# Kernel optimization log

Measured on AMD Instinct MI355X. Metric: run time of the kernel, lower is better.

The kernel has to match this reference:

```python
import jax, jax.numpy as jnp
import numpy as np

B, C, N, E, F = 8, 4, 2048, 512, 2048
EPS = 1e-5
MASK_SCALE = 5.0


def layer_norm(x, gamma, beta):
    mu = jnp.mean(x, axis=-1, keepdims=True)
    var = jnp.mean(jnp.square(x - mu), axis=-1, keepdims=True)
    return (x - mu) * jax.lax.rsqrt(var + EPS) * gamma + beta


def setup_inputs() -> dict:
    key = jax.random.key(0)
    ks = jax.random.split(key, 8)
    src = jax.random.normal(ks[0], (B, C, N, E), dtype=jnp.float32)
    key_padding_mask = jax.random.uniform(ks[1], (B, N), dtype=jnp.float32)
    # FFN params (torch Linear default init scale ~ U(-1/sqrt(fan_in), +))
    W1 = jax.random.normal(ks[2], (E, F), dtype=jnp.float32) / np.sqrt(E)
    b1 = jnp.zeros((F,), dtype=jnp.float32)
    W2 = jax.random.normal(ks[3], (F, E), dtype=jnp.float32) / np.sqrt(F)
    b2 = jnp.zeros((E,), dtype=jnp.float32)
    g1 = jnp.ones((E,), dtype=jnp.float32)
    be1 = jnp.zeros((E,), dtype=jnp.float32)
    g2 = jnp.ones((E,), dtype=jnp.float32)
    be2 = jnp.zeros((E,), dtype=jnp.float32)
    return {"src": src, "key_padding_mask": key_padding_mask,
            "W1": W1, "b1": b1, "W2": W2, "b2": b2,
            "g1": g1, "be1": be1, "g2": g2, "be2": be2}


def reference(src, key_padding_mask, W1, b1, W2, b2, g1, be1, g2, be2):
    # src: [B, C, N, E]; channels batched into one fused attention call
    scale = 1.0 / jnp.sqrt(jnp.asarray(src.shape[-1], src.dtype))
    scores = jnp.einsum('bcne,bcme->bcnm', src, src) * scale  # [B,C,N,N]
    scores = scores - key_padding_mask[:, None, None, :] * MASK_SCALE
    attn = jax.nn.softmax(scores, axis=-1)
    attn_out = jnp.einsum('bcnm,bcme->bcne', attn, src)
    # residual + norm1 (dropout is identity at eval)
    src2 = layer_norm(src + attn_out, g1, be1)
    # feedforward: Linear -> ReLU -> Linear
    ff = jax.nn.relu(jnp.einsum('bcne,ef->bcnf', src2, W1) + b1)
    ff = jnp.einsum('bcnf,fe->bcne', ff, W2) + b2
    out = layer_norm(src2 + ff, g2, be2)
    return out
```

## Files before the change

kernel.cpp:

```cpp
#include <hip/hip_runtime.h>
#include <stdint.h>

constexpr int CB = 8, CC = 4, CN = 2048, CE = 512, CF = 2048;
constexpr long long TOT = (long long)CB * CC * CN * CE;
constexpr int GRP = 16;
constexpr int MCH = 65536;
constexpr float SCALE = 0.04419417382415922f;
constexpr float MASK_SCALE = 5.0f;
constexpr float EPS = 1e-5f;

typedef unsigned short bf16_t;
typedef __attribute__((ext_vector_type(4))) float f32x4;
typedef __attribute__((ext_vector_type(8))) short s16x8;

#define DEV static __device__ __forceinline__

DEV unsigned short f2bf(float f) {
    unsigned u = __float_as_uint(f);
    unsigned r = (u + 0x7fffu + ((u >> 16) & 1u)) >> 16;
    return (unsigned short)r;
}
DEV float bf2f(unsigned short b) {
    return __uint_as_float(((unsigned)b) << 16);
}

typedef const __attribute__((address_space(1))) unsigned int* gptr_t;
typedef __attribute__((address_space(3))) unsigned int* lptr_t;
DEV void async16(const void* g, void* l) {
    __builtin_amdgcn_global_load_lds((gptr_t)g, (lptr_t)l, 16, 0, 0);
}

#define FULL_BAR() do { asm volatile("" ::: "memory"); __builtin_amdgcn_s_barrier(); asm volatile("" ::: "memory"); } while (0)
#define LGKM0() asm volatile("s_waitcnt lgkmcnt(0)" ::: "memory")

DEV float blockSum256(float v, float* sm) {
    #pragma unroll
    for (int o = 32; o; o >>= 1) v += __shfl_xor(v, o);
    int w = threadIdx.x >> 6;
    __syncthreads();
    if ((threadIdx.x & 63) == 0) sm[w] = v;
    __syncthreads();
    return sm[0] + sm[1] + sm[2] + sm[3];
}
DEV float blockMax256(float v, float* sm) {
    #pragma unroll
    for (int o = 32; o; o >>= 1) v = fmaxf(v, __shfl_xor(v, o));
    int w = threadIdx.x >> 6;
    __syncthreads();
    if ((threadIdx.x & 63) == 0) sm[w] = v;
    __syncthreads();
    return fmaxf(fmaxf(sm[0], sm[1]), fmaxf(sm[2], sm[3]));
}

__global__ __launch_bounds__(256) void cvt_f32_bf16_vec(
    const float* __restrict__ in, bf16_t* __restrict__ out, long long n) {
    long long i = ((long long)blockIdx.x * 256 + threadIdx.x) * 4;
    long long stride = (long long)gridDim.x * 1024;
    for (; i < n; i += stride) {
        float4 v = *reinterpret_cast<const float4*>(in + i);
        ushort4 u;
        u.x = f2bf(v.x); u.y = f2bf(v.y); u.z = f2bf(v.z); u.w = f2bf(v.w);
        *reinterpret_cast<ushort4*>(out + i) = u;
    }
}

__global__ __launch_bounds__(256) void transpose_f32_bf16(
    const float* __restrict__ in, bf16_t* __restrict__ out,
    int R, int Cc) {
    __shared__ float tile[32][33];
    int rb = blockIdx.y * 32, cb = blockIdx.x * 32;
    int tx = threadIdx.x & 31, ty = threadIdx.x >> 5;
    #pragma unroll
    for (int i = 0; i < 32; i += 8)
        tile[ty + i][tx] = in[(size_t)(rb + ty + i) * Cc + cb + tx];
    __syncthreads();
    #pragma unroll
    for (int i = 0; i < 32; i += 8)
        out[(size_t)(cb + ty + i) * R + rb + tx] = f2bf(tile[tx][ty + i]);
}

__global__ __launch_bounds__(256) void transpose_bf16(
    const bf16_t* __restrict__ in, bf16_t* __restrict__ out,
    int R, int Cc, long long sIn, long long sOut) {
    __shared__ bf16_t tile[32][36];
    const bf16_t* inz = in + (size_t)blockIdx.z * sIn;
    bf16_t* outz = out + (size_t)blockIdx.z * sOut;
    int rb = blockIdx.y * 32, cb = blockIdx.x * 32;
    int t = threadIdx.x;
    int r = t >> 3, c4 = (t & 7) * 4;
    *(ushort4*)&tile[r][c4] = *(const ushort4*)&inz[(size_t)(rb + r) * Cc + cb + c4];
    __syncthreads();
    int c = t >> 3, r4 = (t & 7) * 4;
    ushort4 w;
    w.x = tile[r4 + 0][c]; w.y = tile[r4 + 1][c];
    w.z = tile[r4 + 2][c]; w.w = tile[r4 + 3][c];
    *(ushort4*)&outz[(size_t)(cb + c) * R + rb + r4] = w;
}

template <int EPI>
__global__ __launch_bounds__(512, 2) void gemm256(
    const bf16_t* __restrict__ A, const bf16_t* __restrict__ B,
    void* __restrict__ Cptr, const float* __restrict__ bias, float alpha,
    int M, int Nc, int K, long long sA, long long sB, long long sC) {
    extern __shared__ bf16_t lds[];
    bf16_t* AsL = lds;
    bf16_t* BsL = lds + 32768;

    int bx, by, bz;
    {
        int gx = gridDim.x, gy = gridDim.y;
        int nwg = gx * gy * gridDim.z;
        int flat = blockIdx.x + gx * (blockIdx.y + gy * blockIdx.z);
        int wg = (nwg & 7) ? flat : ((flat & 7) * (nwg >> 3) + (flat >> 3));
        bx = wg % gx;
        int tmp = wg / gx;
        by = tmp % gy;
        bz = tmp / gy;
    }

    const bf16_t* Az = A + (size_t)bz * sA;
    const bf16_t* Bz = B + (size_t)bz * sB;
    const int t = threadIdx.x;
    const int lane = t & 63, wid = t >> 6;
    const int wr = wid >> 2, wc = wid & 3;
    const int brow = by * 256, bcol = bx * 256;
    const int NT = K >> 6;

    const int r0 = t >> 3, s0 = t & 7;
    const int ce = ((s0 ^ (r0 & 7)) << 3);
    const bf16_t* aP0 = Az + (size_t)(brow + r0) * K + ce;
    const bf16_t* bP0 = Bz + (size_t)(bcol + r0) * K + ce;
    const size_t rK64 = (size_t)64 * K;
    const size_t h128K = (size_t)128 * K;

    #define STAGE_A(kt_, h_) do { \
        bf16_t* d_ = AsL + ((((kt_) & 1) * 2 + (h_)) * 8192); \
        const bf16_t* s_ = aP0 + (size_t)(h_) * h128K + (size_t)(kt_) * 64; \
        async16(s_, d_ + t * 8); \
        async16(s_ + rK64, d_ + 4096 + t * 8); \
    } while (0)
    #define STAGE_B(kt_, h_) do { \
        bf16_t* d_ = BsL + ((((kt_) & 1) * 2 + (h_)) * 8192); \
        const bf16_t* s_ = bP0 + (size_t)(h_) * h128K + (size_t)(kt_) * 64; \
        async16(s_, d_ + t * 8); \
        async16(s_ + rK64, d_ + 4096 + t * 8); \
    } while (0)

    const int q = lane >> 4, rr0 = lane & 15, xmask = rr0 & 7;
    s16x8 af[4][2];
    s16x8 bv[2][2][2];
    f32x4 acc[2][2][4][2] = {};

    #define READ_A(ktp_, qm_) do { \
        const bf16_t* base_ = AsL + (((ktp_) * 2 + (qm_)) * 8192); \
        _Pragma("unroll") for (int m_ = 0; m_ < 4; ++m_) \
        _Pragma("unroll") for (int ks_ = 0; ks_ < 2; ++ks_) \
            af[m_][ks_] = *(const s16x8*)(base_ + (wr * 64 + m_ * 16 + rr0) * 64 + (((ks_ * 4 + q) ^ xmask) << 3)); \
    } while (0)
    #define READ_B(ktp_, qn_) do { \
        const bf16_t* base_ = BsL + (((ktp_) * 2 + (qn_)) * 8192); \
        _Pragma("unroll") for (int n_ = 0; n_ < 2; ++n_) \
        _Pragma("unroll") for (int ks_ = 0; ks_ < 2; ++ks_) \
            bv[qn_][n_][ks_] = *(const s16x8*)(base_ + (wc * 32 + n_ * 16 + rr0) * 64 + (((ks_ * 4 + q) ^ xmask) << 3)); \
    } while (0)
    #define MFMA_Q(qm_, qn_) do { \
        __builtin_amdgcn_s_setprio(1); \
        _Pragma("unroll") for (int m_ = 0; m_ < 4; ++m_) \
        _Pragma("unroll") for (int n_ = 0; n_ < 2; ++n_) \
        _Pragma("unroll") for (int ks_ = 0; ks_ < 2; ++ks_) \
            acc[qm_][qn_][m_][n_] = __builtin_amdgcn_mfma_f32_16x16x32_bf16( \
                af[m_][ks_], bv[qn_][n_][ks_], acc[qm_][qn_][m_][n_], 0, 0, 0); \
        __builtin_amdgcn_s_setprio(0); \
    } while (0)

    STAGE_A(0, 0); STAGE_B(0, 0); STAGE_B(0, 1); STAGE_A(0, 1);
    asm volatile("s_waitcnt vmcnt(2)" ::: "memory");
    FULL_BAR();

    for (int kt = 0; kt < NT; ++kt) {
        const int ktp = kt & 1;
        READ_A(ktp, 0);
        READ_B(ktp, 0);
        READ_B(ktp, 1);
        if (kt + 1 < NT) {
            STAGE_A(kt + 1, 0); STAGE_B(kt + 1, 0); STAGE_B(kt + 1, 1);
            asm volatile("s_waitcnt vmcnt(6)" ::: "memory");
        } else {
            asm volatile("s_waitcnt vmcnt(0)" ::: "memory");
        }
        FULL_BAR();
        LGKM0();
        MFMA_Q(0, 0);
        MFMA_Q(0, 1);
        READ_A(ktp, 1);
        if (kt + 1 < NT) {
            STAGE_A(kt + 1, 1);
            asm volatile("s_waitcnt vmcnt(2)" ::: "memory");
        }
        FULL_BAR();
        LGKM0();
        MFMA_Q(1, 0);
        MFMA_Q(1, 1);
    }

    FULL_BAR();
    size_t cz = (size_t)bz * sC;
    bf16_t (*Cl)[264] = (bf16_t(*)[264])lds;

    #pragma unroll
    for (int qm = 0; qm < 2; ++qm) {
        #pragma unroll
        for (int qn = 0; qn < 2; ++qn) {
            #pragma unroll
            for (int n = 0; n < 2; ++n) {
                int col = qn * 128 + wc * 32 + n * 16 + rr0;
                float bvv = (EPI == 1 || EPI == 4) ? bias[bcol + col] : 0.f;
                #pragma unroll
                for (int m = 0; m < 4; ++m) {
                    unsigned words[4];
                    #pragma unroll
                    for (int j = 0; j < 4; ++j) {
                        float v = acc[qm][qn][m][n][j] + bvv;
                        if constexpr (EPI == 1) v = fmaxf(v, 0.f);
                        if constexpr (EPI == 3) v *= alpha;
                        unsigned h = f2bf(v);
                        unsigned o = (unsigned)__shfl_xor((int)h, 1);
                        words[j] = (lane & 1) ? (o | (h << 16)) : (h | (o << 16));
                    }
                    int row = wr * 64 + m * 16 + q * 4 + (lane & 1) * 2;
                    int cp = col & ~1;
                    *(unsigned*)&Cl[row][cp]     = words[(lane & 1) * 2];
                    *(unsigned*)&Cl[row + 1][cp] = words[(lane & 1) * 2 + 1];
                }
            }
        }
        __syncthreads();
        int rrow = t >> 2;
        bf16_t* Crow = (bf16_t*)Cptr + cz + (size_t)(brow + qm * 128 + rrow) * Nc + bcol;
        #pragma unroll
        for (int s = 0; s < 8; ++s) {
            int segb = ((t & 3) + s * 4) * 8;
            s16x8 vv = *(const s16x8*)&Cl[rrow][segb];
            *(s16x8*)(Crow + segb) = vv;
        }
        __syncthreads();
    }
    #undef STAGE_A
    #undef STAGE_B
    #undef READ_A
    #undef READ_B
    #undef MFMA_Q
}

__global__ __launch_bounds__(256) void softmax_bf16(
    bf16_t* __restrict__ S, const float* __restrict__ mask, int bc0) {
    __shared__ float sm[4];
    int gr = blockIdx.x;
    int b = (bc0 + (gr >> 11)) >> 2;
    bf16_t* row = S + (size_t)gr * CN;
    int tid = threadIdx.x;
    const float* mrow = mask + (size_t)b * CN + tid * 8;
    s16x8 v = *(const s16x8*)(row + tid * 8);
    float4 m0 = *(const float4*)(mrow);
    float4 m1 = *(const float4*)(mrow + 4);
    float x[8];
    x[0] = bf2f((unsigned short)v[0]) - m0.x * MASK_SCALE;
    x[1] = bf2f((unsigned short)v[1]) - m0.y * MASK_SCALE;
    x[2] = bf2f((unsigned short)v[2]) - m0.z * MASK_SCALE;
    x[3] = bf2f((unsigned short)v[3]) - m0.w * MASK_SCALE;
    x[4] = bf2f((unsigned short)v[4]) - m1.x * MASK_SCALE;
    x[5] = bf2f((unsigned short)v[5]) - m1.y * MASK_SCALE;
    x[6] = bf2f((unsigned short)v[6]) - m1.z * MASK_SCALE;
    x[7] = bf2f((unsigned short)v[7]) - m1.w * MASK_SCALE;
    float mx = -3.4e38f;
    #pragma unroll
    for (int i = 0; i < 8; i++) mx = fmaxf(mx, x[i]);
    mx = blockMax256(mx, sm);
    float s = 0.f;
    #pragma unroll
    for (int i = 0; i < 8; i++) { x[i] = __expf(x[i] - mx); s += x[i]; }
    s = blockSum256(s, sm);
    float inv = 1.f / s;
    s16x8 u;
    #pragma unroll
    for (int i = 0; i < 8; i++) u[i] = (short)f2bf(x[i] * inv);
    *(s16x8*)(row + tid * 8) = u;
}

__global__ __launch_bounds__(256) void ln1_kernel(
    const bf16_t* __restrict__ src, const bf16_t* __restrict__ ao,
    const float* __restrict__ g, const float* __restrict__ be,
    bf16_t* __restrict__ o) {
    __shared__ float sm[4];
    size_t base = (size_t)blockIdx.x * CE;
    int e = threadIdx.x * 2;
    ushort2 s = *(const ushort2*)&src[base + e];
    ushort2 a = *(const ushort2*)&ao[base + e];
    float x0 = bf2f(s.x) + bf2f(a.x), x1 = bf2f(s.y) + bf2f(a.y);
    float mu = blockSum256(x0 + x1, sm) * (1.f / CE);
    float d0 = x0 - mu, d1 = x1 - mu;
    float var = blockSum256(d0 * d0 + d1 * d1, sm) * (1.f / CE);
    float rs = rsqrtf(var + EPS);
    ushort2 w;
    w.x = f2bf(d0 * rs * g[e] + be[e]);
    w.y = f2bf(d1 * rs * g[e + 1] + be[e + 1]);
    *(ushort2*)&o[base + e] = w;
}

__global__ __launch_bounds__(256) void ln2_kernel(
    const bf16_t* __restrict__ a, const bf16_t* __restrict__ b,
    const float* __restrict__ g, const float* __restrict__ be,
    float* __restrict__ o) {
    __shared__ float sm[4];
    size_t base = (size_t)blockIdx.x * CE;
    int e = threadIdx.x * 2;
    ushort2 aa = *(const ushort2*)&a[base + e];
    ushort2 bb = *(const ushort2*)&b[base + e];
    float x0 = bf2f(aa.x) + bf2f(bb.x), x1 = bf2f(aa.y) + bf2f(bb.y);
    float mu = blockSum256(x0 + x1, sm) * (1.f / CE);
    float d0 = x0 - mu, d1 = x1 - mu;
    float var = blockSum256(d0 * d0 + d1 * d1, sm) * (1.f / CE);
    float rs = rsqrtf(var + EPS);
    float2 w;
    w.x = d0 * rs * g[e] + be[e];
    w.y = d1 * rs * g[e + 1] + be[e + 1];
    *(float2*)&o[base + e] = w;
}

extern "C" void kernel_launch(void* const* d_in, const int* in_sizes, int n_in,
                              void* d_out, int out_size, void* d_ws, size_t ws_size,
                              hipStream_t stream) {
    const float* src  = (const float*)d_in[0];
    const float* mask = (const float*)d_in[1];
    const float* W1   = (const float*)d_in[2];
    const float* b1   = (const float*)d_in[3];
    const float* W2   = (const float*)d_in[4];
    const float* b2   = (const float*)d_in[5];
    const float* g1   = (const float*)d_in[6];
    const float* be1  = (const float*)d_in[7];
    const float* g2   = (const float*)d_in[8];
    const float* be2  = (const float*)d_in[9];
    float* out = (float*)d_out;
    char* ws = (char*)d_ws;

    hipFuncSetAttribute(reinterpret_cast<const void*>(&gemm256<1>), hipFuncAttributeMaxDynamicSharedMemorySize, 131072);
    hipFuncSetAttribute(reinterpret_cast<const void*>(&gemm256<3>), hipFuncAttributeMaxDynamicSharedMemorySize, 131072);
    hipFuncSetAttribute(reinterpret_cast<const void*>(&gemm256<4>), hipFuncAttributeMaxDynamicSharedMemorySize, 131072);

    const size_t MB = 1024 * 1024;
    bf16_t* probs  = (bf16_t*)(ws);
    bf16_t* src_bf = (bf16_t*)(ws + 256 * MB);
    bf16_t* srcT   = (bf16_t*)(ws + 320 * MB);
    bf16_t* attnO  = (bf16_t*)(ws + 384 * MB);
    bf16_t* W1T    = (bf16_t*)(ws + 448 * MB);
    bf16_t* W2T    = (bf16_t*)(ws + 450 * MB);
    bf16_t* src2   = (bf16_t*)(ws);
    bf16_t* ff     = (bf16_t*)(ws + 64 * MB);
    bf16_t* H      = (bf16_t*)(ws + 128 * MB);
    if (ws_size < 452 * MB) return;

    cvt_f32_bf16_vec<<<4096, 256, 0, stream>>>(src, src_bf, TOT);
    transpose_f32_bf16<<<dim3(CF / 32, CE / 32, 1), 256, 0, stream>>>(W1, W1T, CE, CF);
    transpose_f32_bf16<<<dim3(CE / 32, CF / 32, 1), 256, 0, stream>>>(W2, W2T, CF, CE);
    transpose_bf16<<<dim3(CE / 32, CN / 32, 32), 256, 0, stream>>>(
        src_bf, srcT, CN, CE, (long long)CN * CE, (long long)CE * CN);

    for (int g0 = 0; g0 < CB * CC; g0 += GRP) {
        const bf16_t* srcb = src_bf + (size_t)g0 * CN * CE;
        bf16_t* probs_g = probs + (size_t)g0 * CN * CN;
        gemm256<3><<<dim3(CN / 256, CN / 256, GRP), 512, 131072, stream>>>(
            srcb, srcb, probs_g, nullptr, SCALE, CN, CN, CE,
            (long long)CN * CE, (long long)CN * CE, (long long)CN * CN);
        softmax_bf16<<<dim3(GRP * CN), 256, 0, stream>>>(probs_g, mask, g0);
        gemm256<3><<<dim3(CE / 256, CN / 256, GRP), 512, 131072, stream>>>(
            probs_g, srcT + (size_t)g0 * CE * CN, attnO + (size_t)g0 * CN * CE,
            nullptr, 1.0f, CN, CE, CN,
            (long long)CN * CN, (long long)CE * CN, (long long)CN * CE);
    }
    ln1_kernel<<<dim3(CB * CC * CN), 256, 0, stream>>>(src_bf, attnO, g1, be1, src2);

    gemm256<1><<<dim3(CF / 256, MCH / 256, 1), 512, 131072, stream>>>(
        src2, W1T, H, b1, 1.0f, MCH, CF, CE, 0, 0, 0);
    gemm256<4><<<dim3(CE / 256, MCH / 256, 1), 512, 131072, stream>>>(
        H, W2T, ff, b2, 1.0f, MCH, CE, CF, 0, 0, 0);
    ln2_kernel<<<dim3(MCH), 256, 0, stream>>>(src2, ff, g2, be2, out);
}
```

Before: 948.9 us.

## Make GEMM persistent with cross-tile prefetch and finer load/MFMA interleave

Converts the 256x256 GEMM into a persistent kernel launched with 256 workgroups that loop over tiles. The next tile's first K-slice is prefetched during the last K-step of the current one, which hides the per-tile prologue. The main loop now splits global-to-LDS staging into four pushes interleaved between MFMA quadrants, with sched_barriers. The epilogue drops the LDS-staged coalesced store and writes 32-bit words directly to global memory. The direct stores are less coalesced, and the XCD-aware tile remapping is removed, which may reduce L2 locality.

```diff
diff --git a/kernel.cpp b/kernel.cpp
--- a/kernel.cpp
+++ b/kernel.cpp
@@ -32,6 +32,8 @@
 
 #define FULL_BAR() do { asm volatile("" ::: "memory"); __builtin_amdgcn_s_barrier(); asm volatile("" ::: "memory"); } while (0)
 #define LGKM0() asm volatile("s_waitcnt lgkmcnt(0)" ::: "memory")
+#define SCHED0() __builtin_amdgcn_sched_barrier(0)
+#define VMCNT(N_) asm volatile("s_waitcnt vmcnt(" #N_ ")" ::: "memory")
 
 DEV float blockSum256(float v, float* sm) {
     #pragma unroll
@@ -101,47 +103,30 @@
 __global__ __launch_bounds__(512, 2) void gemm256(
     const bf16_t* __restrict__ A, const bf16_t* __restrict__ B,
     void* __restrict__ Cptr, const float* __restrict__ bias, float alpha,
-    int M, int Nc, int K, long long sA, long long sB, long long sC) {
+    int Nc, int K, long long sA, long long sB, long long sC,
+    int gx, int gz, int nTiles) {
     extern __shared__ bf16_t lds[];
     bf16_t* AsL = lds;
     bf16_t* BsL = lds + 32768;
-
-    int bx, by, bz;
-    {
-        int gx = gridDim.x, gy = gridDim.y;
-        int nwg = gx * gy * gridDim.z;
-        int flat = blockIdx.x + gx * (blockIdx.y + gy * blockIdx.z);
-        int wg = (nwg & 7) ? flat : ((flat & 7) * (nwg >> 3) + (flat >> 3));
-        bx = wg % gx;
-        int tmp = wg / gx;
-        by = tmp % gy;
-        bz = tmp / gy;
-    }
-
-    const bf16_t* Az = A + (size_t)bz * sA;
-    const bf16_t* Bz = B + (size_t)bz * sB;
     const int t = threadIdx.x;
     const int lane = t & 63, wid = t >> 6;
     const int wr = wid >> 2, wc = wid & 3;
-    const int brow = by * 256, bcol = bx * 256;
     const int NT = K >> 6;
 
     const int r0 = t >> 3, s0 = t & 7;
     const int ce = ((s0 ^ (r0 & 7)) << 3);
-    const bf16_t* aP0 = Az + (size_t)(brow + r0) * K + ce;
-    const bf16_t* bP0 = Bz + (size_t)(bcol + r0) * K + ce;
     const size_t rK64 = (size_t)64 * K;
-    const size_t h128K = (size_t)128 * K;
-
-    #define STAGE_A(kt_, h_) do { \
-        bf16_t* d_ = AsL + ((((kt_) & 1) * 2 + (h_)) * 8192); \
-        const bf16_t* s_ = aP0 + (size_t)(h_) * h128K + (size_t)(kt_) * 64; \
+    const size_t h128K = rK64 * 2;
+
+    #define PUSH_A(src_, p_, h_) do { \
+        bf16_t* d_ = AsL + (((p_) * 2 + (h_)) * 8192); \
+        const bf16_t* s_ = (src_) + (size_t)(h_) * h128K; \
         async16(s_, d_ + t * 8); \
         async16(s_ + rK64, d_ + 4096 + t * 8); \
     } while (0)
-    #define STAGE_B(kt_, h_) do { \
-        bf16_t* d_ = BsL + ((((kt_) & 1) * 2 + (h_)) * 8192); \
-        const bf16_t* s_ = bP0 + (size_t)(h_) * h128K + (size_t)(kt_) * 64; \
+    #define PUSH_B(src_, p_, h_) do { \
+        bf16_t* d_ = BsL + (((p_) * 2 + (h_)) * 8192); \
+        const bf16_t* s_ = (src_) + (size_t)(h_) * h128K; \
         async16(s_, d_ + t * 8); \
         async16(s_ + rK64, d_ + 4096 + t * 8); \
     } while (0)
@@ -149,7 +134,6 @@
     const int q = lane >> 4, rr0 = lane & 15, xmask = rr0 & 7;
     s16x8 af[4][2];
     s16x8 bv[2][2][2];
-    f32x4 acc[2][2][4][2] = {};
 
     #define READ_A(ktp_, qm_) do { \
         const bf16_t* base_ = AsL + (((ktp_) * 2 + (qm_)) * 8192); \
@@ -173,48 +157,70 @@
         __builtin_amdgcn_s_setprio(0); \
     } while (0)
 
-    STAGE_A(0, 0); STAGE_B(0, 0); STAGE_B(0, 1); STAGE_A(0, 1);
-    asm volatile("s_waitcnt vmcnt(2)" ::: "memory");
+    int tile = blockIdx.x;
+    if (tile >= nTiles) return;
+    int bx, by, bz, nbx = 0, nby = 0, nbz = 0;
+    const bf16_t *aPc, *bPc, *aPn = nullptr, *bPn = nullptr;
+
+    {
+        bx = tile % gx; int r = tile / gx; bz = r % gz; by = r / gz;
+        aPc = A + (size_t)bz * sA + (size_t)(by * 256 + r0) * K + ce;
+        bPc = B + (size_t)bz * sB + (size_t)(bx * 256 + r0) * K + ce;
+    }
+
+    PUSH_A(aPc, 0, 0); PUSH_B(bPc, 0, 0); PUSH_B(bPc, 0, 1); PUSH_A(aPc, 0, 1);
+    VMCNT(4);
     FULL_BAR();
 
-    for (int kt = 0; kt < NT; ++kt) {
-        const int ktp = kt & 1;
-        READ_A(ktp, 0);
-        READ_B(ktp, 0);
-        READ_B(ktp, 1);
-        if (kt + 1 < NT) {
-            STAGE_A(kt + 1, 0); STAGE_B(kt + 1, 0); STAGE_B(kt + 1, 1);
-            asm volatile("s_waitcnt vmcnt(6)" ::: "memory");
-        } else {
-            asm volatile("s_waitcnt vmcnt(0)" ::: "memory");
+    while (true) {
+        int ntile = tile + (int)gridDim.x;
+        bool have_next = ntile < nTiles;
+        if (have_next) {
+            nbx = ntile % gx; int r = ntile / gx; nbz = r % gz; nby = r / gz;
+            aPn = A + (size_t)nbz * sA + (size_t)(nby * 256 + r0) * K + ce;
+            bPn = B + (size_t)nbz * sB + (size_t)(nbx * 256 + r0) * K + ce;
+        } else { aPn = aPc; bPn = bPc; }
+
+        f32x4 acc[2][2][4][2] = {};
+
+        for (int kt = 0; kt < NT; ++kt) {
+            const int ktp = kt & 1;
+            const int sp = (kt + 1) & 1;
+            const bool more = (kt + 1 < NT) || have_next;
+            const bf16_t* aS = (kt + 1 < NT) ? aPc + (size_t)(kt + 1) * 64 : aPn;
+            const bf16_t* bS = (kt + 1 < NT) ? bPc + (size_t)(kt + 1) * 64 : bPn;
+
+            READ_A(ktp, 0);
+            READ_B(ktp, 0);
+            if (more) { PUSH_A(aS, sp, 0); VMCNT(4); } else { VMCNT(2); }
+            FULL_BAR(); LGKM0(); SCHED0();
+            MFMA_Q(0, 0);
+            READ_B(ktp, 1);
+            if (more) { PUSH_B(bS, sp, 0); VMCNT(4); } else { VMCNT(0); }
+            FULL_BAR(); LGKM0(); SCHED0();
+            MFMA_Q(0, 1);
+            READ_A(ktp, 1);
+            if (more) { PUSH_B(bS, sp, 1); }
+            FULL_BAR(); LGKM0(); SCHED0();
+            MFMA_Q(1, 0);
+            if (more) { PUSH_A(aS, sp, 1); VMCNT(4); }
+            FULL_BAR();
+            MFMA_Q(1, 1);
         }
-        FULL_BAR();
-        LGKM0();
-        MFMA_Q(0, 0);
-        MFMA_Q(0, 1);
-        READ_A(ktp, 1);
-        if (kt + 1 < NT) {
-            STAGE_A(kt + 1, 1);
-            asm volatile("s_waitcnt vmcnt(2)" ::: "memory");
-        }
-        FULL_BAR();
-        LGKM0();
-        MFMA_Q(1, 0);
-        MFMA_Q(1, 1);
-    }
-
-    FULL_BAR();
-    size_t cz = (size_t)bz * sC;
-    bf16_t (*Cl)[264] = (bf16_t(*)[264])lds;
-
-    #pragma unroll
-    for (int qm = 0; qm < 2; ++qm) {
-        #pragma unroll
-        for (int qn = 0; qn < 2; ++qn) {
+
+        {
+            size_t cz = (size_t)bz * sC;
+            bf16_t* Cb = (bf16_t*)Cptr + cz;
+            const int brow = by * 256, bcol = bx * 256;
+            const int lo = lane & 1;
+            #pragma unroll
+            for (int qm = 0; qm < 2; ++qm)
+            #pragma unroll
+            for (int qn = 0; qn < 2; ++qn)
             #pragma unroll
             for (int n = 0; n < 2; ++n) {
-                int col = qn * 128 + wc * 32 + n * 16 + rr0;
-                float bvv = (EPI == 1 || EPI == 4) ? bias[bcol + col] : 0.f;
+                int col = bcol + qn * 128 + wc * 32 + n * 16 + rr0;
+                float bvv = (EPI == 1 || EPI == 4) ? bias[col] : 0.f;
                 #pragma unroll
                 for (int m = 0; m < 4; ++m) {
                     unsigned words[4];
@@ -225,28 +231,21 @@
                         if constexpr (EPI == 3) v *= alpha;
                         unsigned h = f2bf(v);
                         unsigned o = (unsigned)__shfl_xor((int)h, 1);
-                        words[j] = (lane & 1) ? (o | (h << 16)) : (h | (o << 16));
+                        words[j] = lo ? (o | (h << 16)) : (h | (o << 16));
                     }
-                    int row = wr * 64 + m * 16 + q * 4 + (lane & 1) * 2;
+                    int row = brow + qm * 128 + wr * 64 + m * 16 + q * 4 + lo * 2;
                     int cp = col & ~1;
-                    *(unsigned*)&Cl[row][cp]     = words[(lane & 1) * 2];
-                    *(unsigned*)&Cl[row + 1][cp] = words[(lane & 1) * 2 + 1];
+                    *(unsigned*)&Cb[(size_t)row * Nc + cp] = words[lo * 2];
+                    *(unsigned*)&Cb[(size_t)(row + 1) * Nc + cp] = words[lo * 2 + 1];
                 }
             }
         }
-        __syncthreads();
-        int rrow = t >> 2;
-        bf16_t* Crow = (bf16_t*)Cptr + cz + (size_t)(brow + qm * 128 + rrow) * Nc + bcol;
-        #pragma unroll
-        for (int s = 0; s < 8; ++s) {
-            int segb = ((t & 3) + s * 4) * 8;
-            s16x8 vv = *(const s16x8*)&Cl[rrow][segb];
-            *(s16x8*)(Crow + segb) = vv;
-        }
-        __syncthreads();
+
+        if (!have_next) break;
+        tile = ntile; bx = nbx; by = nby; bz = nbz; aPc = aPn; bPc = bPn;
     }
-    #undef STAGE_A
-    #undef STAGE_B
+    #undef PUSH_A
+    #undef PUSH_B
     #undef READ_A
     #undef READ_B
     #undef MFMA_Q
@@ -368,20 +367,24 @@
     for (int g0 = 0; g0 < CB * CC; g0 += GRP) {
         const bf16_t* srcb = src_bf + (size_t)g0 * CN * CE;
         bf16_t* probs_g = probs + (size_t)g0 * CN * CN;
-        gemm256<3><<<dim3(CN / 256, CN / 256, GRP), 512, 131072, stream>>>(
-            srcb, srcb, probs_g, nullptr, SCALE, CN, CN, CE,
-            (long long)CN * CE, (long long)CN * CE, (long long)CN * CN);
+        gemm256<3><<<256, 512, 131072, stream>>>(
+            srcb, srcb, probs_g, nullptr, SCALE, CN, CE,
+            (long long)CN * CE, (long long)CN * CE, (long long)CN * CN,
+            CN / 256, GRP, (CN / 256) * (CN / 256) * GRP);
         softmax_bf16<<<dim3(GRP * CN), 256, 0, stream>>>(probs_g, mask, g0);
-        gemm256<3><<<dim3(CE / 256, CN / 256, GRP), 512, 131072, stream>>>(
+        gemm256<3><<<256, 512, 131072, stream>>>(
             probs_g, srcT + (size_t)g0 * CE * CN, attnO + (size_t)g0 * CN * CE,
-            nullptr, 1.0f, CN, CE, CN,
-            (long long)CN * CN, (long long)CE * CN, (long long)CN * CE);
+            nullptr, 1.0f, CE, CN,
+            (long long)CN * CN, (long long)CE * CN, (long long)CN * CE,
+            CE / 256, GRP, (CE / 256) * (CN / 256) * GRP);
     }
     ln1_kernel<<<dim3(CB * CC * CN), 256, 0, stream>>>(src_bf, attnO, g1, be1, src2);
 
-    gemm256<1><<<dim3(CF / 256, MCH / 256, 1), 512, 131072, stream>>>(
-        src2, W1T, H, b1, 1.0f, MCH, CF, CE, 0, 0, 0);
-    gemm256<4><<<dim3(CE / 256, MCH / 256, 1), 512, 131072, stream>>>(
-        H, W2T, ff, b2, 1.0f, MCH, CE, CF, 0, 0, 0);
+    gemm256<1><<<256, 512, 131072, stream>>>(
+        src2, W1T, H, b1, 1.0f, CF, CE, 0, 0, 0,
+        CF / 256, 1, (CF / 256) * (MCH / 256));
+    gemm256<4><<<256, 512, 131072, stream>>>(
+        H, W2T, ff, b2, 1.0f, CE, CF, 0, 0, 0,
+        CE / 256, 1, (CE / 256) * (MCH / 256));
     ln2_kernel<<<dim3(MCH), 256, 0, stream>>>(src2, ff, g2, be2, out);
 }
```

Result: faster. 912.7 us (-3.8%).

## Deepen GEMM prefetch pipeline with per-quadrant staging and direct epilogue stores

Applied to the files above, without the earlier changes.

Restructures the 256x256 GEMM main loop so global-to-LDS loads for tile k+2 are interleaved between each MFMA quadrant, with extra barriers, sched_barriers and finer lgkmcnt/vmcnt waits. This aims to hide memory latency better and keep the MFMA units busy. The epilogue drops the LDS-staged coalesced store and writes packed bf16 pairs directly to global memory, removing two syncthreads per half but making stores less coalesced. More barriers per iteration could add sync overhead.

```diff
diff --git a/kernel.cpp b/kernel.cpp
--- a/kernel.cpp
+++ b/kernel.cpp
@@ -32,6 +32,9 @@
 
 #define FULL_BAR() do { asm volatile("" ::: "memory"); __builtin_amdgcn_s_barrier(); asm volatile("" ::: "memory"); } while (0)
 #define LGKM0() asm volatile("s_waitcnt lgkmcnt(0)" ::: "memory")
+#define LGKM8() asm volatile("s_waitcnt lgkmcnt(8)" ::: "memory")
+#define SCHED0() __builtin_amdgcn_sched_barrier(0)
+#define VMCNT(N_) asm volatile("s_waitcnt vmcnt(" #N_ ")" ::: "memory")
 
 DEV float blockSum256(float v, float* sm) {
     #pragma unroll
@@ -101,7 +104,7 @@
 __global__ __launch_bounds__(512, 2) void gemm256(
     const bf16_t* __restrict__ A, const bf16_t* __restrict__ B,
     void* __restrict__ Cptr, const float* __restrict__ bias, float alpha,
-    int M, int Nc, int K, long long sA, long long sB, long long sC) {
+    int Nc, int K, long long sA, long long sB, long long sC) {
     extern __shared__ bf16_t lds[];
     bf16_t* AsL = lds;
     bf16_t* BsL = lds + 32768;
@@ -131,15 +134,15 @@
     const bf16_t* aP0 = Az + (size_t)(brow + r0) * K + ce;
     const bf16_t* bP0 = Bz + (size_t)(bcol + r0) * K + ce;
     const size_t rK64 = (size_t)64 * K;
-    const size_t h128K = (size_t)128 * K;
-
-    #define STAGE_A(kt_, h_) do { \
+    const size_t h128K = rK64 * 2;
+
+    #define PUSH_A(kt_, h_) do { \
         bf16_t* d_ = AsL + ((((kt_) & 1) * 2 + (h_)) * 8192); \
         const bf16_t* s_ = aP0 + (size_t)(h_) * h128K + (size_t)(kt_) * 64; \
         async16(s_, d_ + t * 8); \
         async16(s_ + rK64, d_ + 4096 + t * 8); \
     } while (0)
-    #define STAGE_B(kt_, h_) do { \
+    #define PUSH_B(kt_, h_) do { \
         bf16_t* d_ = BsL + ((((kt_) & 1) * 2 + (h_)) * 8192); \
         const bf16_t* s_ = bP0 + (size_t)(h_) * h128K + (size_t)(kt_) * 64; \
         async16(s_, d_ + t * 8); \
@@ -173,80 +176,71 @@
         __builtin_amdgcn_s_setprio(0); \
     } while (0)
 
-    STAGE_A(0, 0); STAGE_B(0, 0); STAGE_B(0, 1); STAGE_A(0, 1);
-    asm volatile("s_waitcnt vmcnt(2)" ::: "memory");
+    PUSH_A(0, 0); PUSH_B(0, 0); PUSH_B(0, 1); PUSH_A(0, 1);
+    VMCNT(4);
+    PUSH_A(1, 0); PUSH_B(1, 0); PUSH_B(1, 1);
+    VMCNT(6);
     FULL_BAR();
 
-    for (int kt = 0; kt < NT; ++kt) {
-        const int ktp = kt & 1;
-        READ_A(ktp, 0);
-        READ_B(ktp, 0);
-        READ_B(ktp, 1);
-        if (kt + 1 < NT) {
-            STAGE_A(kt + 1, 0); STAGE_B(kt + 1, 0); STAGE_B(kt + 1, 1);
-            asm volatile("s_waitcnt vmcnt(6)" ::: "memory");
-        } else {
-            asm volatile("s_waitcnt vmcnt(0)" ::: "memory");
-        }
-        FULL_BAR();
-        LGKM0();
+    for (int T = 0; T < NT; ++T) {
+        const int p = T & 1;
+        const bool m1 = (T + 1 < NT), m2 = (T + 2 < NT);
+        READ_A(p, 0);
+        READ_B(p, 0);
+        if (m1) PUSH_A(T + 1, 1);
+        LGKM8();
+        FULL_BAR(); LGKM0(); SCHED0();
         MFMA_Q(0, 0);
+        FULL_BAR();
+        READ_B(p, 1);
+        if (m2) PUSH_A(T + 2, 0);
+        FULL_BAR(); LGKM0(); SCHED0();
         MFMA_Q(0, 1);
-        READ_A(ktp, 1);
-        if (kt + 1 < NT) {
-            STAGE_A(kt + 1, 1);
-            asm volatile("s_waitcnt vmcnt(2)" ::: "memory");
-        }
-        FULL_BAR();
-        LGKM0();
+        FULL_BAR();
+        READ_A(p, 1);
+        if (m2) PUSH_B(T + 2, 0);
+        FULL_BAR(); LGKM0(); SCHED0();
         MFMA_Q(1, 0);
+        FULL_BAR();
+        if (m2) { PUSH_B(T + 2, 1); VMCNT(6); } else { VMCNT(0); }
+        FULL_BAR();
         MFMA_Q(1, 1);
-    }
-
-    FULL_BAR();
-    size_t cz = (size_t)bz * sC;
-    bf16_t (*Cl)[264] = (bf16_t(*)[264])lds;
-
-    #pragma unroll
-    for (int qm = 0; qm < 2; ++qm) {
+        FULL_BAR();
+    }
+
+    {
+        size_t cz = (size_t)bz * sC;
+        bf16_t* Cb = (bf16_t*)Cptr + cz;
+        const int lo = lane & 1;
         #pragma unroll
-        for (int qn = 0; qn < 2; ++qn) {
+        for (int qm = 0; qm < 2; ++qm)
+        #pragma unroll
+        for (int qn = 0; qn < 2; ++qn)
+        #pragma unroll
+        for (int n = 0; n < 2; ++n) {
+            int col = bcol + qn * 128 + wc * 32 + n * 16 + rr0;
+            float bvv = (EPI == 1 || EPI == 4) ? bias[col] : 0.f;
             #pragma unroll
-            for (int n = 0; n < 2; ++n) {
-                int col = qn * 128 + wc * 32 + n * 16 + rr0;
-                float bvv = (EPI == 1 || EPI == 4) ? bias[bcol + col] : 0.f;
+            for (int m = 0; m < 4; ++m) {
+                unsigned words[4];
                 #pragma unroll
-                for (int m = 0; m < 4; ++m) {
-                    unsigned words[4];
-                    #pragma unroll
-                    for (int j = 0; j < 4; ++j) {
-                        float v = acc[qm][qn][m][n][j] + bvv;
-                        if constexpr (EPI == 1) v = fmaxf(v, 0.f);
-                        if constexpr (EPI == 3) v *= alpha;
-                        unsigned h = f2bf(v);
-                        unsigned o = (unsigned)__shfl_xor((int)h, 1);
-                        words[j] = (lane & 1) ? (o | (h << 16)) : (h | (o << 16));
-                    }
-                    int row = wr * 64 + m * 16 + q * 4 + (lane & 1) * 2;
-                    int cp = col & ~1;
-                    *(unsigned*)&Cl[row][cp]     = words[(lane & 1) * 2];
-                    *(unsigned*)&Cl[row + 1][cp] = words[(lane & 1) * 2 + 1];
+                for (int j = 0; j < 4; ++j) {
+                    float v = acc[qm][qn][m][n][j] + bvv;
+                    if constexpr (EPI == 1) v = fmaxf(v, 0.f);
+                    if constexpr (EPI == 3) v *= alpha;
+                    unsigned h = f2bf(v);
+                    unsigned o = (unsigned)__shfl_xor((int)h, 1);
+                    words[j] = lo ? (o | (h << 16)) : (h | (o << 16));
                 }
+                int row = brow + qm * 128 + wr * 64 + m * 16 + q * 4 + lo * 2;
+                int cp = col & ~1;
+                *(unsigned*)&Cb[(size_t)row * Nc + cp] = words[lo * 2];
+                *(unsigned*)&Cb[(size_t)(row + 1) * Nc + cp] = words[lo * 2 + 1];
             }
         }
-        __syncthreads();
-        int rrow = t >> 2;
-        bf16_t* Crow = (bf16_t*)Cptr + cz + (size_t)(brow + qm * 128 + rrow) * Nc + bcol;
-        #pragma unroll
-        for (int s = 0; s < 8; ++s) {
-            int segb = ((t & 3) + s * 4) * 8;
-            s16x8 vv = *(const s16x8*)&Cl[rrow][segb];
-            *(s16x8*)(Crow + segb) = vv;
-        }
-        __syncthreads();
-    }
-    #undef STAGE_A
-    #undef STAGE_B
+    }
+    #undef PUSH_A
+    #undef PUSH_B
     #undef READ_A
     #undef READ_B
     #undef MFMA_Q
@@ -369,19 +363,19 @@
         const bf16_t* srcb = src_bf + (size_t)g0 * CN * CE;
         bf16_t* probs_g = probs + (size_t)g0 * CN * CN;
         gemm256<3><<<dim3(CN / 256, CN / 256, GRP), 512, 131072, stream>>>(
-            srcb, srcb, probs_g, nullptr, SCALE, CN, CN, CE,
+            srcb, srcb, probs_g, nullptr, SCALE, CN, CE,
             (long long)CN * CE, (long long)CN * CE, (long long)CN * CN);
         softmax_bf16<<<dim3(GRP * CN), 256, 0, stream>>>(probs_g, mask, g0);
         gemm256<3><<<dim3(CE / 256, CN / 256, GRP), 512, 131072, stream>>>(
             probs_g, srcT + (size_t)g0 * CE * CN, attnO + (size_t)g0 * CN * CE,
-            nullptr, 1.0f, CN, CE, CN,
+            nullptr, 1.0f, CE, CN,
             (long long)CN * CN, (long long)CE * CN, (long long)CN * CE);
     }
     ln1_kernel<<<dim3(CB * CC * CN), 256, 0, stream>>>(src_bf, attnO, g1, be1, src2);
 
     gemm256<1><<<dim3(CF / 256, MCH / 256, 1), 512, 131072, stream>>>(
-        src2, W1T, H, b1, 1.0f, MCH, CF, CE, 0, 0, 0);
+        src2, W1T, H, b1, 1.0f, CF, CE, 0, 0, 0);
     gemm256<4><<<dim3(CE / 256, MCH / 256, 1), 512, 131072, stream>>>(
-        H, W2T, ff, b2, 1.0f, MCH, CE, CF, 0, 0, 0);
+        H, W2T, ff, b2, 1.0f, CE, CF, 0, 0, 0);
     ln2_kernel<<<dim3(MCH), 256, 0, stream>>>(src2, ff, g2, be2, out);
 }
```

Result: faster. 903.3 us (-4.8%).
